# Kernel tuning notes

Hardware: AMD Instinct MI355X
Metric: run time of the kernel (lower is better)

Reference implementation:

```python
import jax, jax.numpy as jnp
import numpy as np

V, E, H = 32000, 256, 512  # vocab, embedding_size, hidden_size
B, T = 64, 512             # batch, seq_len


def setup_inputs() -> dict:
    key = jax.random.key(0)
    ks = jax.random.split(key, 8)
    inputs = jax.random.randint(ks[0], (B, T), 0, V)
    lengths = jax.random.randint(ks[1], (B,), 0, T)
    reset_indices = jax.random.randint(ks[2], (B, T), 0, 2, dtype=jnp.int32)
    # nn.Embedding: N(0,1) init with padding_idx row zeroed
    emb = jax.random.normal(ks[3], (V, E), dtype=jnp.float32).at[0].set(0.0)
    # nn.LSTMCell params: uniform(-1/sqrt(H), 1/sqrt(H)), gate order i,f,g,o
    s = 1.0 / np.sqrt(H)
    W_ih = jax.random.uniform(ks[4], (4 * H, E), minval=-s, maxval=s, dtype=jnp.float32)
    W_hh = jax.random.uniform(ks[5], (4 * H, H), minval=-s, maxval=s, dtype=jnp.float32)
    b_ih = jax.random.uniform(ks[6], (4 * H,), minval=-s, maxval=s, dtype=jnp.float32)
    b_hh = jax.random.uniform(ks[7], (4 * H,), minval=-s, maxval=s, dtype=jnp.float32)
    return {"inputs": inputs, "lengths": lengths, "reset_indices": reset_indices,
            "emb": emb, "W_ih": W_ih, "W_hh": W_hh, "b_ih": b_ih, "b_hh": b_hh}


def reference(inputs, lengths, reset_indices, emb, W_ih, W_hh, b_ih, b_hh):
    x = emb[inputs]                                        # (B,T,E); dropout is identity in eval
    mask = (jnp.arange(T) < lengths[:, None]).astype(x.dtype)   # (B,T) length mask
    xt = jnp.swapaxes(x, 0, 1)                             # (T,B,E) time-major
    m_t = mask.T                                           # (T,B)
    r_t = reset_indices.astype(x.dtype).T                  # (T,B)
    # precompute input contribution to gates for all timesteps
    gates_x = jnp.einsum('tbe,ge->tbg', xt, W_ih) + b_ih + b_hh  # (T,B,4H)

    def step(carry, inp):
        h, c = carry
        gx, m, r = inp
        g = gx + h @ W_hh.T                                # (B,4H)
        i, f, gg, o = jnp.split(g, 4, axis=-1)
        i = jax.nn.sigmoid(i); f = jax.nn.sigmoid(f)
        gg = jnp.tanh(gg); o = jax.nn.sigmoid(o)
        c_new = f * c + i * gg
        h_new = o * jnp.tanh(c_new)
        mm = m[:, None]; rr = r[:, None]
        h_next = h_new * mm + h * (1 - mm)                 # mask-blend (keep state past length)
        c_next = c_new * mm + c * (1 - mm)
        # reset zeroing applied to carried state AFTER output is recorded
        return (h_next * (1 - rr), c_next * (1 - rr)), h_next

    h0 = jnp.zeros((B, H), dtype=x.dtype)
    (hT, cT), out_t = jax.lax.scan(step, (h0, h0), (gates_x, m_t, r_t))  # out_t: (T,B,H)
    output = jnp.swapaxes(out_t, 0, 1)                     # (B,T,H) = output.transpose(0,1)
    return output, hT, cT, mask
```

## Files before the change

### kernel.cpp

```cpp
#include <hip/hip_runtime.h>
#include <stdint.h>
#include <stddef.h>

constexpr int V = 32000, E = 256, H = 512, B = 64, T = 512;
constexpr int NTHR = 512;
constexpr int NBLK = 64;
constexpr int BATG = 16;
constexpr int HPB = 32;

constexpr int PSW = 128 * 17;
constexpr int OFF_PS   = 0;
constexpr int OFF_BIAS = OFF_PS + 8 * PSW * 4;
constexpr int OFF_LEN  = OFF_BIAS + 128 * 4;
constexpr int LDS_BYTES = 84 * 1024;

constexpr size_t OUT_HT   = (size_t)B * T * H;
constexpr size_t OUT_CT   = OUT_HT + (size_t)B * H;
constexpr size_t OUT_MASK = OUT_CT + (size_t)B * H;

typedef __attribute__((ext_vector_type(8))) short short8;
typedef __attribute__((ext_vector_type(4))) float f32x4;
typedef __attribute__((ext_vector_type(4))) unsigned int u32x4;

__device__ __forceinline__ unsigned short f2bf(float f) {
  uint32_t u = __builtin_bit_cast(uint32_t, f);
  return (unsigned short)((u + 0x7fffu + ((u >> 16) & 1u)) >> 16);
}
__device__ __forceinline__ short8 pack_bf8(float4 v0, float4 v1) {
  short8 r;
  r[0] = (short)f2bf(v0.x); r[1] = (short)f2bf(v0.y);
  r[2] = (short)f2bf(v0.z); r[3] = (short)f2bf(v0.w);
  r[4] = (short)f2bf(v1.x); r[5] = (short)f2bf(v1.y);
  r[6] = (short)f2bf(v1.z); r[7] = (short)f2bf(v1.w);
  return r;
}
__device__ __forceinline__ float sigmoidf_fast(float x) {
  return 1.f / (1.f + __expf(-x));
}
__device__ __forceinline__ float tanhf_fast(float x) {
  return 1.f - 2.f / (__expf(2.f * x) + 1.f);
}
__device__ __forceinline__ void st_word(uint32_t* p, uint32_t v) {
  __hip_atomic_store(p, v, __ATOMIC_RELAXED, __HIP_MEMORY_SCOPE_AGENT);
}
__device__ __forceinline__ void ld_mall_k64(const uint32_t* p, u32x4& r0,
                                            u32x4& r1, u32x4& r2, u32x4& r3) {
  asm volatile(
      "global_load_dwordx4 %0, %4, off sc1\n\t"
      "global_load_dwordx4 %1, %4, off offset:16 sc1\n\t"
      "global_load_dwordx4 %2, %4, off offset:128 sc1\n\t"
      "global_load_dwordx4 %3, %4, off offset:144 sc1\n\t"
      "s_waitcnt vmcnt(0)"
      : "=&v"(r0), "=&v"(r1), "=&v"(r2), "=&v"(r3)
      : "v"(p)
      : "memory");
}
__device__ __forceinline__ short8 cvt_frag(u32x4 lo, u32x4 hi) {
  uint32_t d0, d1, d2, d3;
  asm("v_cvt_pk_bf16_f32 %0, %1, %2" : "=v"(d0) : "v"(lo[0]), "v"(lo[1]));
  asm("v_cvt_pk_bf16_f32 %0, %1, %2" : "=v"(d1) : "v"(lo[2]), "v"(lo[3]));
  asm("v_cvt_pk_bf16_f32 %0, %1, %2" : "=v"(d2) : "v"(hi[0]), "v"(hi[1]));
  asm("v_cvt_pk_bf16_f32 %0, %1, %2" : "=v"(d3) : "v"(hi[2]), "v"(hi[3]));
  u32x4 d = {d0, d1, d2, d3};
  return __builtin_bit_cast(short8, d);
}

__global__ void __launch_bounds__(NTHR, 1)
lstm_mfma(const int* __restrict__ inputs, const int* __restrict__ lengths,
          const int* __restrict__ resets, const float* __restrict__ emb,
          const float* __restrict__ W_ih, const float* __restrict__ W_hh,
          const float* __restrict__ b_ih, const float* __restrict__ b_hh,
          float* __restrict__ out, uint32_t* __restrict__ hw) {
  extern __shared__ char lds[];
  float* Ps = (float*)(lds + OFF_PS);
  float* Bias = (float*)(lds + OFF_BIAS);
  int* Lens = (int*)(lds + OFF_LEN);

  const int tid = threadIdx.x;
  const int blk = blockIdx.x;
  const int grp = blk & 3;
  const int rq = blk >> 2;
  const int khid = rq * HPB;
  const int b0 = grp * BATG;

  const int w = tid >> 6;
  const int L = tid & 63;
  const int lc = L & 15;
  const int q = L >> 4;

  short8 wfh[2][8];
  short8 wfe[8];
  #pragma unroll
  for (int s = 0; s < 2; ++s) {
    #pragma unroll
    for (int tl = 0; tl < 8; ++tl) {
      const int n = 16 * tl + lc;
      const int grow = (n >> 5) * H + khid + (n & 31);
      const float* src = W_hh + (size_t)grow * H + 64 * w + 32 * s + 8 * q;
      wfh[s][tl] = pack_bf8(*(const float4*)src, *(const float4*)(src + 4));
    }
  }
  #pragma unroll
  for (int tl = 0; tl < 8; ++tl) {
    const int n = 16 * tl + lc;
    const int grow = (n >> 5) * H + khid + (n & 31);
    const float* src = W_ih + (size_t)grow * E + 32 * w + 8 * q;
    wfe[tl] = pack_bf8(*(const float4*)src, *(const float4*)(src + 4));
  }
  if (tid < 128) {
    const int grow = (tid >> 5) * H + khid + (tid & 31);
    Bias[tid] = b_ih[grow] + b_hh[grow];
  }
  if (tid < 16) Lens[tid] = lengths[b0 + tid];
  {
    int i = blk * 512 + tid;
    int mb = i >> 9, mt = i & (T - 1);
    out[OUT_MASK + i] = (mt < lengths[mb]) ? 1.f : 0.f;
  }
  __syncthreads();

  const int jj = tid & 31;
  const int bb = tid >> 5;

  float carry_h = 0.f, carry_c = 0.f;

  for (int t = 0; t < T; ++t) {
    const uint32_t* hsrc = hw + (size_t)(t & 1) * (B * H);
    uint32_t* hdst = hw + (size_t)((t + 1) & 1) * (B * H);

    float rr = (float)resets[(b0 + bb) * T + t];
    const int tok = inputs[(b0 + lc) * T + t];
    const float* eb = emb + (size_t)tok * E + 32 * w + 8 * q;
    short8 ae = pack_bf8(*(const float4*)eb, *(const float4*)(eb + 4));
    f32x4 acc[8];
    const f32x4 zero4 = {0.f, 0.f, 0.f, 0.f};
    #pragma unroll
    for (int tl = 0; tl < 8; ++tl)
      acc[tl] = __builtin_amdgcn_mfma_f32_16x16x32_bf16(ae, wfe[tl], zero4, 0, 0, 0);

    if (t > 0) {
      const uint32_t expect = 4u | (((uint32_t)(t - 1) >> 1) & 3u);
      const uint32_t* p = hsrc + (size_t)(b0 + lc) * H + 64 * w + 8 * q;
      u32x4 r0, r1, r2, r3;
      for (;;) {
        ld_mall_k64(p, r0, r1, r2, r3);
        uint32_t o = (r0[0] | r0[1] | r0[2] | r0[3]) |
                     (r1[0] | r1[1] | r1[2] | r1[3]) |
                     (r2[0] | r2[1] | r2[2] | r2[3]) |
                     (r3[0] | r3[1] | r3[2] | r3[3]);
        uint32_t a = (r0[0] & r0[1] & r0[2] & r0[3]) &
                     (r1[0] & r1[1] & r1[2] & r1[3]) &
                     (r2[0] & r2[1] & r2[2] & r2[3]) &
                     (r3[0] & r3[1] & r3[2] & r3[3]);
        uint32_t bad = ((o ^ expect) | (a ^ expect)) & 7u;
        if (!__any((int)bad)) break;
      }
      short8 a0 = cvt_frag(r0, r1);
      short8 a1 = cvt_frag(r2, r3);
      #pragma unroll
      for (int tl = 0; tl < 8; ++tl)
        acc[tl] = __builtin_amdgcn_mfma_f32_16x16x32_bf16(a0, wfh[0][tl], acc[tl], 0, 0, 0);
      #pragma unroll
      for (int tl = 0; tl < 8; ++tl)
        acc[tl] = __builtin_amdgcn_mfma_f32_16x16x32_bf16(a1, wfh[1][tl], acc[tl], 0, 0, 0);
    }

    #pragma unroll
    for (int tl = 0; tl < 8; ++tl)
      *(f32x4*)(Ps + w * PSW + (16 * tl + lc) * 17 + 4 * q) = acc[tl];
    __syncthreads();

    float g4[4];
    #pragma unroll
    for (int gi = 0; gi < 4; ++gi) {
      const int n = gi * 32 + jj;
      float s = Bias[n];
      #pragma unroll
      for (int ww = 0; ww < 8; ++ww) s += Ps[ww * PSW + n * 17 + bb];
      g4[gi] = s;
    }
    __syncthreads();

    float ig = sigmoidf_fast(g4[0]);
    float fg = sigmoidf_fast(g4[1]);
    float gg = tanhf_fast(g4[2]);
    float og = sigmoidf_fast(g4[3]);
    float c_new = fg * carry_c + ig * gg;
    float h_new = og * tanhf_fast(c_new);
    bool live = (t < Lens[bb]);
    float h_next = live ? h_new : carry_h;
    float c_next = live ? c_new : carry_c;
    carry_h = h_next * (1.f - rr);
    carry_c = c_next * (1.f - rr);

    if (t < T - 1) {
      const uint32_t wtag = 4u | (((uint32_t)t >> 1) & 3u);
      uint32_t bits = (__builtin_bit_cast(uint32_t, carry_h) & ~7u) | wtag;
      st_word(hdst + (size_t)(b0 + bb) * H + HPB * rq + jj, bits);
    }
    out[((size_t)(b0 + bb) * T + t) * H + khid + jj] = h_next;
  }
  out[OUT_HT + (size_t)(b0 + bb) * H + khid + jj] = carry_h;
  out[OUT_CT + (size_t)(b0 + bb) * H + khid + jj] = carry_c;
}

extern "C" void kernel_launch(void* const* d_in, const int* in_sizes, int n_in,
                              void* d_out, int out_size, void* d_ws, size_t ws_size,
                              hipStream_t stream) {
  const int* inputs    = (const int*)d_in[0];
  const int* lengths   = (const int*)d_in[1];
  const int* resets    = (const int*)d_in[2];
  const float* emb     = (const float*)d_in[3];
  const float* W_ih    = (const float*)d_in[4];
  const float* W_hh    = (const float*)d_in[5];
  const float* b_ih    = (const float*)d_in[6];
  const float* b_hh    = (const float*)d_in[7];
  float* out = (float*)d_out;

  uint32_t* hw = (uint32_t*)d_ws;

  hipFuncSetAttribute((const void*)lstm_mfma,
                      hipFuncAttributeMaxDynamicSharedMemorySize, LDS_BYTES);

  hipMemsetAsync(d_ws, 0, (size_t)2 * B * H * 4, stream);
  lstm_mfma<<<NBLK, NTHR, LDS_BYTES, stream>>>(
      inputs, lengths, resets, emb, W_ih, W_hh, b_ih, b_hh, out, hw);
}
```

Before: 2.088 ms.

## Exchange hidden state through L2 with a MALL fallback buffer

Launches 128 blocks and keeps only those with grp<4, so that with round-robin XCD dispatch each batch group's 16 cooperating blocks are meant to share one XCD and its L2. The hidden state is written twice, once to an L2-coherent buffer and once with sc1 to a MALL-visible buffer. Readers poll the L2 copy with sc0 loads and switch permanently to the MALL copy after 64 failed spins. This aims to cut the cross-block handoff latency on every timestep. It relies on an assumed block-to-XCD mapping and adds a second store per step, and if the mapping assumption fails the fallback path costs extra spinning.

```diff
diff --git a/kernel.cpp b/kernel.cpp
--- a/kernel.cpp
+++ b/kernel.cpp
@@ -4,7 +4,7 @@
 
 constexpr int V = 32000, E = 256, H = 512, B = 64, T = 512;
 constexpr int NTHR = 512;
-constexpr int NBLK = 64;
+constexpr int NBLK = 128;
 constexpr int BATG = 16;
 constexpr int HPB = 32;
 
@@ -40,8 +40,25 @@
 __device__ __forceinline__ float tanhf_fast(float x) {
   return 1.f - 2.f / (__expf(2.f * x) + 1.f);
 }
-__device__ __forceinline__ void st_word(uint32_t* p, uint32_t v) {
-  __hip_atomic_store(p, v, __ATOMIC_RELAXED, __HIP_MEMORY_SCOPE_AGENT);
+__device__ __forceinline__ void st_h_dual(uint32_t* pl2, uint32_t* pml,
+                                          uint32_t v) {
+  asm volatile(
+      "global_store_dword %0, %2, off\n\t"
+      "global_store_dword %1, %2, off sc1"
+      :: "v"(pl2), "v"(pml), "v"(v)
+      : "memory");
+}
+__device__ __forceinline__ void ld_l2_k64(const uint32_t* p, u32x4& r0,
+                                          u32x4& r1, u32x4& r2, u32x4& r3) {
+  asm volatile(
+      "global_load_dwordx4 %0, %4, off sc0\n\t"
+      "global_load_dwordx4 %1, %4, off offset:16 sc0\n\t"
+      "global_load_dwordx4 %2, %4, off offset:128 sc0\n\t"
+      "global_load_dwordx4 %3, %4, off offset:144 sc0\n\t"
+      "s_waitcnt vmcnt(0)"
+      : "=&v"(r0), "=&v"(r1), "=&v"(r2), "=&v"(r3)
+      : "v"(p)
+      : "memory");
 }
 __device__ __forceinline__ void ld_mall_k64(const uint32_t* p, u32x4& r0,
                                             u32x4& r1, u32x4& r2, u32x4& r3) {
@@ -70,7 +87,8 @@
           const int* __restrict__ resets, const float* __restrict__ emb,
           const float* __restrict__ W_ih, const float* __restrict__ W_hh,
           const float* __restrict__ b_ih, const float* __restrict__ b_hh,
-          float* __restrict__ out, uint32_t* __restrict__ hw) {
+          float* __restrict__ out, uint32_t* __restrict__ hL2,
+          uint32_t* __restrict__ hML) {
   extern __shared__ char lds[];
   float* Ps = (float*)(lds + OFF_PS);
   float* Bias = (float*)(lds + OFF_BIAS);
@@ -78,8 +96,10 @@
 
   const int tid = threadIdx.x;
   const int blk = blockIdx.x;
-  const int grp = blk & 3;
-  const int rq = blk >> 2;
+  const int grp = blk & 7;
+  if (grp >= 4) return;
+  const int rq = blk >> 3;
+  const int vblk = grp * 16 + rq;
   const int khid = rq * HPB;
   const int b0 = grp * BATG;
 
@@ -113,7 +133,7 @@
   }
   if (tid < 16) Lens[tid] = lengths[b0 + tid];
   {
-    int i = blk * 512 + tid;
+    int i = vblk * 512 + tid;
     int mb = i >> 9, mt = i & (T - 1);
     out[OUT_MASK + i] = (mt < lengths[mb]) ? 1.f : 0.f;
   }
@@ -123,10 +143,11 @@
   const int bb = tid >> 5;
 
   float carry_h = 0.f, carry_c = 0.f;
+  bool fb = false;
 
   for (int t = 0; t < T; ++t) {
-    const uint32_t* hsrc = hw + (size_t)(t & 1) * (B * H);
-    uint32_t* hdst = hw + (size_t)((t + 1) & 1) * (B * H);
+    const size_t srcbase = (size_t)(t & 1) * (B * H);
+    const size_t dstbase = (size_t)((t + 1) & 1) * (B * H);
 
     float rr = (float)resets[(b0 + bb) * T + t];
     const int tok = inputs[(b0 + lc) * T + t];
@@ -140,10 +161,14 @@
 
     if (t > 0) {
       const uint32_t expect = 4u | (((uint32_t)(t - 1) >> 1) & 3u);
-      const uint32_t* p = hsrc + (size_t)(b0 + lc) * H + 64 * w + 8 * q;
+      const size_t off = srcbase + (size_t)(b0 + lc) * H + 64 * w + 8 * q;
+      const uint32_t* pl2 = hL2 + off;
+      const uint32_t* pml = hML + off;
       u32x4 r0, r1, r2, r3;
+      int spins = 0;
       for (;;) {
-        ld_mall_k64(p, r0, r1, r2, r3);
+        if (!fb) ld_l2_k64(pl2, r0, r1, r2, r3);
+        else     ld_mall_k64(pml, r0, r1, r2, r3);
         uint32_t o = (r0[0] | r0[1] | r0[2] | r0[3]) |
                      (r1[0] | r1[1] | r1[2] | r1[3]) |
                      (r2[0] | r2[1] | r2[2] | r2[3]) |
@@ -154,6 +179,7 @@
                      (r3[0] & r3[1] & r3[2] & r3[3]);
         uint32_t bad = ((o ^ expect) | (a ^ expect)) & 7u;
         if (!__any((int)bad)) break;
+        if (!fb && ++spins >= 64) fb = true;
       }
       short8 a0 = cvt_frag(r0, r1);
       short8 a1 = cvt_frag(r2, r3);
@@ -196,7 +222,8 @@
     if (t < T - 1) {
       const uint32_t wtag = 4u | (((uint32_t)t >> 1) & 3u);
       uint32_t bits = (__builtin_bit_cast(uint32_t, carry_h) & ~7u) | wtag;
-      st_word(hdst + (size_t)(b0 + bb) * H + HPB * rq + jj, bits);
+      const size_t doff = dstbase + (size_t)(b0 + bb) * H + HPB * rq + jj;
+      st_h_dual(hL2 + doff, hML + doff, bits);
     }
     out[((size_t)(b0 + bb) * T + t) * H + khid + jj] = h_next;
   }
@@ -217,12 +244,14 @@
   const float* b_hh    = (const float*)d_in[7];
   float* out = (float*)d_out;
 
-  uint32_t* hw = (uint32_t*)d_ws;
+  constexpr size_t HBYTES = (size_t)2 * B * H * 4;
+  uint32_t* hL2 = (uint32_t*)d_ws;
+  uint32_t* hML = (uint32_t*)((char*)d_ws + HBYTES);
 
   hipFuncSetAttribute((const void*)lstm_mfma,
                       hipFuncAttributeMaxDynamicSharedMemorySize, LDS_BYTES);
 
-  hipMemsetAsync(d_ws, 0, (size_t)2 * B * H * 4, stream);
+  hipMemsetAsync(d_ws, 0, 2 * HBYTES, stream);
   lstm_mfma<<<NBLK, NTHR, LDS_BYTES, stream>>>(
-      inputs, lengths, resets, emb, W_ih, W_hh, b_ih, b_hh, out, hw);
-}
+      inputs, lengths, resets, emb, W_ih, W_hh, b_ih, b_hh, out, hL2, hML);
+}
```

After: 2.110 ms. Within noise of the previous version (+1.0%).
